# Performance work log

Hardware: AMD Instinct MI355X
Metric: run time of the kernel (lower is better)

The kernel has to match this reference:

```python
import jax, jax.numpy as jnp
import numpy as np

R = 1          # box filter radius -> 3x3 kernel
EPS = 0.01     # regularization


def _box_kernel(r, ch):
    k = 2 * r + 1
    return jnp.full((ch, 1, k, k), 1.0 / (k * k), dtype=jnp.float32)


def _box(x, kernel, groups):
    # depthwise box filter, stride 1, 'same' padding (NCHW)
    return jax.lax.conv_general_dilated(
        x, kernel, window_strides=(1, 1), padding='SAME',
        dimension_numbers=('NCHW', 'OIHW', 'NCHW'),
        feature_group_count=groups)


def setup_inputs() -> dict:
    key = jax.random.key(0)
    k1, k2 = jax.random.split(key)
    shape = (8, 3, 1024, 1024)
    return {
        'x': jax.random.normal(k1, shape, dtype=jnp.float32),
        'y': jax.random.normal(k2, shape, dtype=jnp.float32),
    }


def reference(x, y):
    _, C, H, W = x.shape
    kC = _box_kernel(R, C)   # per-channel depthwise kernel
    k1 = _box_kernel(R, 1)   # normalization kernel
    # N counts valid pixels under 'same' (zero) padding -> edge correction
    Nrm = _box(jnp.ones((1, 1, H, W), x.dtype), k1, 1)
    mean_x = _box(x, kC, C) / Nrm
    mean_y = _box(y, kC, C) / Nrm
    cov_xy = _box(x * y, kC, C) / Nrm - mean_x * mean_y
    var_x = _box(x * x, kC, C) / Nrm - mean_x * mean_x
    A = cov_xy / (var_x + EPS)
    b = mean_y - A * mean_x
    mean_A = _box(A, kC, C) / Nrm
    mean_b = _box(b, kC, C) / Nrm
    return mean_A * x + mean_b
```

## Files before the change

kernel.cpp:

```cpp
#include <hip/hip_runtime.h>


#define H 1024
#define W 1024
#define STRIP 16
#define WAVES 4
#define WVC 256

__device__ __forceinline__ float dpp_up1(float v) {
    return __int_as_float(__builtin_amdgcn_update_dpp(
        0, __float_as_int(v), 0x138 , 0xf, 0xf, true));
}
__device__ __forceinline__ float dpp_dn1(float v) {
    return __int_as_float(__builtin_amdgcn_update_dpp(
        0, __float_as_int(v), 0x130 , 0xf, 0xf, true));
}

__global__ __launch_bounds__(256, 3) void gf_kernel(const float* __restrict__ xg,
                                                    const float* __restrict__ yg,
                                                    float* __restrict__ og)
{
    const int lane = threadIdx.x & 63;
    const int wv = threadIdx.x >> 6;
    const int c0 = blockIdx.x * WVC;
    const int R0 = (blockIdx.y * WAVES + wv) * STRIP;
    const size_t base = (size_t)blockIdx.z * (size_t)(H * W);
    const float* __restrict__ xp = xg + base;
    const float* __restrict__ yp = yg + base;
    float* __restrict__ op = og + base;

    const int colA = c0 + 4 * lane;
    const bool isL = (lane == 0);
    const bool isR = (lane == 63);
    const bool haloIn = isL ? (c0 > 0) : (isR ? (c0 + WVC < W) : false);
    const int hoff = (isL ? (c0 - 2) : (c0 + WVC)) - colA;

    const float third = 1.0f / 3.0f;
    float invc[4];
    invc[0] = (colA == 0) ? 0.5f : third;
    invc[1] = third;
    invc[2] = third;
    invc[3] = (colA + 3 == W - 1) ? 0.5f : third;
    const float invcH = haloIn ? third : 0.0f;

    float pX[4] = {0,0,0,0}, rX[4] = {0,0,0,0};
    float pY[4] = {0,0,0,0}, rY[4] = {0,0,0,0};
    float pXX[4] = {0,0,0,0}, rXX[4] = {0,0,0,0};
    float pXY[4] = {0,0,0,0}, rXY[4] = {0,0,0,0};
    float pHX[2] = {0,0}, rHX[2] = {0,0};
    float pHY[2] = {0,0}, rHY[2] = {0,0};
    float pHXX[2] = {0,0}, rHXX[2] = {0,0};
    float pHXY[2] = {0,0}, rHXY[2] = {0,0};
    float pA[4] = {0,0,0,0}, rA[4] = {0,0,0,0};
    float pB[4] = {0,0,0,0}, rB[4] = {0,0,0,0};
    float pAH = 0, rAH = 0, pBH = 0, rBH = 0;

    int off = (R0 - 2) * W + colA;

    float4 xv = {0,0,0,0}, yv = {0,0,0,0};
    float2 xh = {0,0}, yh = {0,0};
    if (R0 - 2 >= 0) {
        xv = *(const float4*)(xp + off);
        yv = *(const float4*)(yp + off);
        if (haloIn) {
            xh = *(const float2*)(xp + off + hoff);
            yh = *(const float2*)(yp + off + hoff);
        }
    }

#pragma unroll 2
    for (int s = 0; s < STRIP + 4; ++s) {
        const int lr = R0 - 2 + s;
        const int t = lr - 1;
        const int r = lr - 2;

        const int lrn = lr + 1;
        float4 xvN = {0,0,0,0}, yvN = {0,0,0,0};
        float2 xhN = {0,0}, yhN = {0,0};
        if ((unsigned)lrn < (unsigned)H && s < STRIP + 3) {
            const int offn = off + W;
            xvN = *(const float4*)(xp + offn);
            yvN = *(const float4*)(yp + offn);
            if (haloIn) {
                xhN = *(const float2*)(xp + offn + hoff);
                yhN = *(const float2*)(yp + offn + hoff);
            }
        }

        const float x_[4] = {xv.x, xv.y, xv.z, xv.w};
        const float y_[4] = {yv.x, yv.y, yv.z, yv.w};
        float vX[4], vY[4], vXX[4], vXY[4];
#pragma unroll
        for (int c = 0; c < 4; ++c) {
            const float xx = x_[c] * x_[c];
            const float xy = x_[c] * y_[c];
            vX[c]  = pX[c]  + x_[c]; pX[c]  = rX[c]  + x_[c]; rX[c]  = x_[c];
            vY[c]  = pY[c]  + y_[c]; pY[c]  = rY[c]  + y_[c]; rY[c]  = y_[c];
            vXX[c] = pXX[c] + xx;    pXX[c] = rXX[c] + xx;    rXX[c] = xx;
            vXY[c] = pXY[c] + xy;    pXY[c] = rXY[c] + xy;    rXY[c] = xy;
        }
        const float xh_[2] = {xh.x, xh.y};
        const float yh_[2] = {yh.x, yh.y};
        float vHX[2], vHY[2], vHXX[2], vHXY[2];
#pragma unroll
        for (int c = 0; c < 2; ++c) {
            const float xx = xh_[c] * xh_[c];
            const float xy = xh_[c] * yh_[c];
            vHX[c]  = pHX[c]  + xh_[c]; pHX[c]  = rHX[c]  + xh_[c]; rHX[c]  = xh_[c];
            vHY[c]  = pHY[c]  + yh_[c]; pHY[c]  = rHY[c]  + yh_[c]; rHY[c]  = yh_[c];
            vHXX[c] = pHXX[c] + xx;     pHXX[c] = rHXX[c] + xx;     rHXX[c] = xx;
            vHXY[c] = pHXY[c] + xy;     pHXY[c] = rHXY[c] + xy;     rHXY[c] = xy;
        }

        float lX  = dpp_up1(vX[3]),  rXs  = dpp_dn1(vX[0]);
        float lY  = dpp_up1(vY[3]),  rYs  = dpp_dn1(vY[0]);
        float lXX = dpp_up1(vXX[3]), rXXs = dpp_dn1(vXX[0]);
        float lXY = dpp_up1(vXY[3]), rXYs = dpp_dn1(vXY[0]);
        lX  = isL ? vHX[1]  : lX;   rXs  = isR ? vHX[0]  : rXs;
        lY  = isL ? vHY[1]  : lY;   rYs  = isR ? vHY[0]  : rYs;
        lXX = isL ? vHXX[1] : lXX;  rXXs = isR ? vHXX[0] : rXXs;
        lXY = isL ? vHXY[1] : lXY;  rXYs = isR ? vHXY[0] : rXYs;

        float hX[4], hY[4], hXX[4], hXY[4];
        {
            const float s01 = vX[0] + vX[1], s12 = vX[1] + vX[2], s23 = vX[2] + vX[3];
            hX[0] = lX + s01; hX[1] = s01 + vX[2]; hX[2] = s12 + vX[3]; hX[3] = s23 + rXs;
        }
        {
            const float s01 = vY[0] + vY[1], s12 = vY[1] + vY[2], s23 = vY[2] + vY[3];
            hY[0] = lY + s01; hY[1] = s01 + vY[2]; hY[2] = s12 + vY[3]; hY[3] = s23 + rYs;
        }
        {
            const float s01 = vXX[0] + vXX[1], s12 = vXX[1] + vXX[2], s23 = vXX[2] + vXX[3];
            hXX[0] = lXX + s01; hXX[1] = s01 + vXX[2]; hXX[2] = s12 + vXX[3]; hXX[3] = s23 + rXXs;
        }
        {
            const float s01 = vXY[0] + vXY[1], s12 = vXY[1] + vXY[2], s23 = vXY[2] + vXY[3];
            hXY[0] = lXY + s01; hXY[1] = s01 + vXY[2]; hXY[2] = s12 + vXY[3]; hXY[3] = s23 + rXYs;
        }

        const float rowfA = ((unsigned)t >= (unsigned)H) ? 0.0f
                          : ((t == 0 || t == H - 1) ? 0.5f : third);
        float A_[4], B_[4];
#pragma unroll
        for (int c = 0; c < 4; ++c) {
            const float ic  = rowfA * invc[c];
            const float mx  = hX[c]  * ic;
            const float my  = hY[c]  * ic;
            const float mxx = hXX[c] * ic;
            const float mxy = hXY[c] * ic;
            const float var = fmaf(-mx, mx, mxx);
            const float cov = fmaf(-mx, my, mxy);
            A_[c] = cov * __builtin_amdgcn_rcpf(var + 0.01f);
            B_[c] = fmaf(-A_[c], mx, my);
        }
        float AH, BH;
        {
            const float iH  = rowfA * invcH;
            const float hx  = vHX[0]  + vHX[1]  + (isL ? vX[0]  : vX[3]);
            const float hy  = vHY[0]  + vHY[1]  + (isL ? vY[0]  : vY[3]);
            const float hxx = vHXX[0] + vHXX[1] + (isL ? vXX[0] : vXX[3]);
            const float hxy = vHXY[0] + vHXY[1] + (isL ? vXY[0] : vXY[3]);
            const float mx  = hx * iH, my = hy * iH, mxx = hxx * iH, mxy = hxy * iH;
            const float var = fmaf(-mx, mx, mxx);
            const float cov = fmaf(-mx, my, mxy);
            AH = cov * __builtin_amdgcn_rcpf(var + 0.01f);
            BH = fmaf(-AH, mx, my);
        }

        float vA[4], vB[4];
#pragma unroll
        for (int c = 0; c < 4; ++c) {
            vA[c] = pA[c] + A_[c]; pA[c] = rA[c] + A_[c]; rA[c] = A_[c];
            vB[c] = pB[c] + B_[c]; pB[c] = rB[c] + B_[c]; rB[c] = B_[c];
        }
        const float vAH = pAH + AH;  pAH = rAH + AH;  rAH = AH;
        const float vBH = pBH + BH;  pBH = rBH + BH;  rBH = BH;

        float lA = dpp_up1(vA[3]), rAs = dpp_dn1(vA[0]);
        float lB = dpp_up1(vB[3]), rBs = dpp_dn1(vB[0]);
        lA = isL ? vAH : lA;  rAs = isR ? vAH : rAs;
        lB = isL ? vBH : lB;  rBs = isR ? vBH : rBs;

        if (s >= 4) {
            float hA[4], hB[4];
            {
                const float s01 = vA[0] + vA[1], s12 = vA[1] + vA[2], s23 = vA[2] + vA[3];
                hA[0] = lA + s01; hA[1] = s01 + vA[2]; hA[2] = s12 + vA[3]; hA[3] = s23 + rAs;
            }
            {
                const float s01 = vB[0] + vB[1], s12 = vB[1] + vB[2], s23 = vB[2] + vB[3];
                hB[0] = lB + s01; hB[1] = s01 + vB[2]; hB[2] = s12 + vB[3]; hB[3] = s23 + rBs;
            }
            const float rowfO = (r == 0 || r == H - 1) ? 0.5f : third;
            float4 o;
            float o_[4];
#pragma unroll
            for (int c = 0; c < 4; ++c) {
                const float oc = rowfO * invc[c];
                const float xc = vX[c] - pX[c];
                o_[c] = fmaf(hA[c] * oc, xc, hB[c] * oc);
            }
            o.x = o_[0]; o.y = o_[1]; o.z = o_[2]; o.w = o_[3];
            *(float4*)(op + (off - 2 * W)) = o;
        }

        xv = xvN; yv = yvN; xh = xhN; yh = yhN;
        off += W;
    }
}

extern "C" void kernel_launch(void* const* d_in, const int* in_sizes, int n_in,
                              void* d_out, int out_size, void* d_ws, size_t ws_size,
                              hipStream_t stream) {
    const float* x = (const float*)d_in[0];
    const float* y = (const float*)d_in[1];
    float* out = (float*)d_out;
    const int planes = in_sizes[0] / (H * W);
    dim3 grid(W / WVC, H / (STRIP * WAVES), planes);
    gf_kernel<<<grid, dim3(256), 0, stream>>>(x, y, out);
}
```

Baseline: 254.2 us.

## Stage input rows through LDS with async global_load_lds triple buffering

```diff
diff --git a/kernel.cpp b/kernel.cpp
--- a/kernel.cpp
+++ b/kernel.cpp
@@ -7,6 +7,9 @@
 #define WAVES 4
 #define WVC 256
 
+typedef const void __attribute__((address_space(1)))* gas1_t;
+typedef void __attribute__((address_space(3)))* las3_t;
+
 __device__ __forceinline__ float dpp_up1(float v) {
     return __int_as_float(__builtin_amdgcn_update_dpp(
         0, __float_as_int(v), 0x138 , 0xf, 0xf, true));
@@ -20,6 +23,8 @@
                                                     const float* __restrict__ yg,
                                                     float* __restrict__ og)
 {
+    __shared__ float lds[WAVES][3][2][264];
+
     const int lane = threadIdx.x & 63;
     const int wv = threadIdx.x >> 6;
     const int c0 = blockIdx.x * WVC;
@@ -33,7 +38,9 @@
     const bool isL = (lane == 0);
     const bool isR = (lane == 63);
     const bool haloIn = isL ? (c0 > 0) : (isR ? (c0 + WVC < W) : false);
-    const int hoff = (isL ? (c0 - 2) : (c0 + WVC)) - colA;
+
+    int hc = (lane < 2) ? (c0 - 2 + lane) : (c0 + WVC + (lane - 2));
+    hc = hc < 0 ? 0 : (hc > W - 1 ? W - 1 : hc);
 
     const float third = 1.0f / 3.0f;
     float invc[4];
@@ -55,18 +62,30 @@
     float pB[4] = {0,0,0,0}, rB[4] = {0,0,0,0};
     float pAH = 0, rAH = 0, pBH = 0, rBH = 0;
 
-    int off = (R0 - 2) * W + colA;
-
-    float4 xv = {0,0,0,0}, yv = {0,0,0,0};
-    float2 xh = {0,0}, yh = {0,0};
-    if (R0 - 2 >= 0) {
-        xv = *(const float4*)(xp + off);
-        yv = *(const float4*)(yp + off);
-        if (haloIn) {
-            xh = *(const float2*)(xp + off + hoff);
-            yh = *(const float2*)(yp + off + hoff);
-        }
+    auto stage = [&](int row, int slot) {
+        const int rb = row * W;
+        __builtin_amdgcn_global_load_lds((gas1_t)(xp + rb + colA),
+                                         (las3_t)&lds[wv][slot][0][0], 16, 0, 0);
+        __builtin_amdgcn_global_load_lds((gas1_t)(yp + rb + colA),
+                                         (las3_t)&lds[wv][slot][1][0], 16, 0, 0);
+        if (lane < 4) {
+            __builtin_amdgcn_global_load_lds((gas1_t)(xp + rb + hc),
+                                             (las3_t)&lds[wv][slot][0][256], 4, 0, 0);
+            __builtin_amdgcn_global_load_lds((gas1_t)(yp + rb + hc),
+                                             (las3_t)&lds[wv][slot][1][256], 4, 0, 0);
+        }
+    };
+
+    {
+        int r0 = R0 - 2; r0 = r0 < 0 ? 0 : r0;
+        int r1 = R0 - 1; r1 = r1 < 0 ? 0 : r1;
+        stage(r0, 0);
+        stage(r1, 1);
     }
+
+    int slotC = 0;
+    int slotS = 2;
+    int offSt = (R0 - 4) * W + colA;
 
 #pragma unroll 2
     for (int s = 0; s < STRIP + 4; ++s) {
@@ -74,21 +93,28 @@
         const int t = lr - 1;
         const int r = lr - 2;
 
-        const int lrn = lr + 1;
-        float4 xvN = {0,0,0,0}, yvN = {0,0,0,0};
-        float2 xhN = {0,0}, yhN = {0,0};
-        if ((unsigned)lrn < (unsigned)H && s < STRIP + 3) {
-            const int offn = off + W;
-            xvN = *(const float4*)(xp + offn);
-            yvN = *(const float4*)(yp + offn);
-            if (haloIn) {
-                xhN = *(const float2*)(xp + offn + hoff);
-                yhN = *(const float2*)(yp + offn + hoff);
-            }
-        }
-
-        const float x_[4] = {xv.x, xv.y, xv.z, xv.w};
-        const float y_[4] = {yv.x, yv.y, yv.z, yv.w};
+        {
+            int rs = R0 + s; rs = rs < H ? rs : H - 1;
+            stage(rs, slotS);
+        }
+
+        asm volatile("s_waitcnt vmcnt(8)" ::: "memory");
+
+        const bool rowv = ((unsigned)lr < (unsigned)H);
+        const float4 xv4 = *(const float4*)&lds[wv][slotC][0][4 * lane];
+        const float4 yv4 = *(const float4*)&lds[wv][slotC][1][4 * lane];
+        const int hsel = isR ? 258 : 256;
+        const float2 xh2 = *(const float2*)&lds[wv][slotC][0][hsel];
+        const float2 yh2 = *(const float2*)&lds[wv][slotC][1][hsel];
+
+        const float x_[4] = { rowv ? xv4.x : 0.0f, rowv ? xv4.y : 0.0f,
+                              rowv ? xv4.z : 0.0f, rowv ? xv4.w : 0.0f };
+        const float y_[4] = { rowv ? yv4.x : 0.0f, rowv ? yv4.y : 0.0f,
+                              rowv ? yv4.z : 0.0f, rowv ? yv4.w : 0.0f };
+        const bool hv = haloIn && rowv;
+        const float xh_[2] = { hv ? xh2.x : 0.0f, hv ? xh2.y : 0.0f };
+        const float yh_[2] = { hv ? yh2.x : 0.0f, hv ? yh2.y : 0.0f };
+
         float vX[4], vY[4], vXX[4], vXY[4];
 #pragma unroll
         for (int c = 0; c < 4; ++c) {
@@ -99,8 +125,6 @@
             vXX[c] = pXX[c] + xx;    pXX[c] = rXX[c] + xx;    rXX[c] = xx;
             vXY[c] = pXY[c] + xy;    pXY[c] = rXY[c] + xy;    rXY[c] = xy;
         }
-        const float xh_[2] = {xh.x, xh.y};
-        const float yh_[2] = {yh.x, yh.y};
         float vHX[2], vHY[2], vHXX[2], vHXY[2];
 #pragma unroll
         for (int c = 0; c < 2; ++c) {
@@ -202,11 +226,12 @@
                 o_[c] = fmaf(hA[c] * oc, xc, hB[c] * oc);
             }
             o.x = o_[0]; o.y = o_[1]; o.z = o_[2]; o.w = o_[3];
-            *(float4*)(op + (off - 2 * W)) = o;
-        }
-
-        xv = xvN; yv = yvN; xh = xhN; yh = yhN;
-        off += W;
+            *(float4*)(op + offSt) = o;
+        }
+
+        slotC = (slotC == 2) ? 0 : slotC + 1;
+        slotS = (slotS == 2) ? 0 : slotS + 1;
+        offSt += W;
     }
 }
 
```

Measured after the change: 257.7 us. No clear change (+1.4%).
